# Kernel tuning notes

Hardware: AMD Instinct MI355X
Metric: run time of the kernel (lower is better)

Reference implementation:

```python
import jax, jax.numpy as jnp
import numpy as np

PADDING = 300
NMS_THRESH = 0.5


def bbox_transform_inv(boxes, deltas):
    # boxes: (N,4) x1,y1,x2,y2 ; deltas: (N,4*C) -> (N,4*C) decoded boxes
    w = boxes[:, 2] - boxes[:, 0] + 1.0
    h = boxes[:, 3] - boxes[:, 1] + 1.0
    cx = boxes[:, 0] + 0.5 * w
    cy = boxes[:, 1] + 0.5 * h
    dx, dy = deltas[:, 0::4], deltas[:, 1::4]
    dw, dh = deltas[:, 2::4], deltas[:, 3::4]
    pcx = dx * w[:, None] + cx[:, None]
    pcy = dy * h[:, None] + cy[:, None]
    pw = jnp.exp(dw) * w[:, None]
    ph = jnp.exp(dh) * h[:, None]
    out = jnp.stack([pcx - 0.5 * pw, pcy - 0.5 * ph,
                     pcx + 0.5 * pw, pcy + 0.5 * ph], axis=2)  # (N,C,4)
    return out.reshape(boxes.shape[0], -1)


def clip_boxes(boxes, hw):
    # hw = (H, W); boxes (N, 4*C)
    b = boxes.reshape(boxes.shape[0], -1, 4)
    x1 = jnp.clip(b[..., 0], 0.0, hw[1] - 1.0)
    y1 = jnp.clip(b[..., 1], 0.0, hw[0] - 1.0)
    x2 = jnp.clip(b[..., 2], 0.0, hw[1] - 1.0)
    y2 = jnp.clip(b[..., 3], 0.0, hw[0] - 1.0)
    return jnp.stack([x1, y1, x2, y2], axis=2).reshape(boxes.shape[0], -1)


def nms(boxes, scores, max_out, thresh):
    # Greedy NMS: sequential argmax + IoU suppression (fixed max_out iters).
    N = boxes.shape[0]
    x1, y1, x2, y2 = boxes[:, 0], boxes[:, 1], boxes[:, 2], boxes[:, 3]
    areas = (x2 - x1 + 1.0) * (y2 - y1 + 1.0)
    neg_inf = jnp.array(-jnp.inf, boxes.dtype)

    def step(s, _):
        i = jnp.argmax(s)
        valid = s[i] > neg_inf
        xx1 = jnp.maximum(x1[i], x1)
        yy1 = jnp.maximum(y1[i], y1)
        xx2 = jnp.minimum(x2[i], x2)
        yy2 = jnp.minimum(y2[i], y2)
        inter = jnp.maximum(xx2 - xx1 + 1.0, 0.0) * jnp.maximum(yy2 - yy1 + 1.0, 0.0)
        iou = inter / (areas[i] + areas - inter)
        suppress = (iou > thresh) | (jnp.arange(N) == i)
        s = jnp.where(suppress, neg_inf, s)
        return s, (i, valid)

    _, (idx, valid) = jax.lax.scan(step, scores, None, length=max_out)
    return idx, valid


def reference(metadata, deltas, proposals, scores, masks):
    N = proposals.shape[1]
    C = scores.shape[2]
    prop = proposals.reshape(-1, 4)
    boxes = prop / metadata[0, 2]                       # undo image scale
    d = deltas.reshape(N, -1)
    pred = bbox_transform_inv(boxes, d)                 # (N, 4C)
    pred = clip_boxes(pred, metadata[0, :2])
    sc = scores.reshape(N, C)
    top = jnp.argmax(sc, axis=1)                        # most probable class
    predc = pred.reshape(N, C, 4)
    pbox = jnp.take_along_axis(predc, top[:, None, None], axis=1)[:, 0, :]  # (N,4)
    max_scores = jnp.max(sc[:, 1:], axis=1)             # skip background col
    idx, valid = nms(jax.lax.stop_gradient(pbox),
                     jax.lax.stop_gradient(max_scores), PADDING, NMS_THRESH)
    vf = valid.astype(pbox.dtype)
    out_boxes = pbox[idx] * vf[:, None]                 # (300,4), zero padded
    out_scores = sc[idx] * vf[:, None]                  # (300,C)
    out_masks = masks[0][idx] * vf[:, None, None, None] # (300,mh,mw,mc)
    return out_boxes[None], out_scores[None], out_masks[None]


def setup_inputs() -> dict:
    key = jax.random.key(0)
    k1, k2, k3, k4, k5 = jax.random.split(key, 5)
    N, C, MH, MW, MC = 6000, 81, 14, 14, 81
    H, W, SCALE = 600.0, 800.0, 1.6
    metadata = jnp.array([[H, W, SCALE]], dtype=jnp.float32)
    # proposals: valid boxes inside the scaled image
    xy = jax.random.uniform(k1, (N, 2), jnp.float32) * jnp.array([W - 120.0, H - 120.0], jnp.float32)
    wh = jax.random.uniform(k2, (N, 2), jnp.float32) * 100.0 + 16.0
    proposals = jnp.concatenate([xy, xy + wh], axis=1)[None] * SCALE  # (1,N,4)
    deltas = jax.random.normal(k3, (1, N, 4 * C), jnp.float32) * 0.1
    scores = jax.random.uniform(k4, (1, N, C), jnp.float32)
    masks = jax.random.uniform(k5, (1, N, MH, MW, MC), jnp.float32)
    return {"metadata": metadata, "deltas": deltas, "proposals": proposals,
            "scores": scores, "masks": masks}
```

## Files before the change

### kernel.cpp

```cpp
#include <hip/hip_runtime.h>
#include <math.h>

#pragma STDC FP_CONTRACT OFF

#define N 6000
#define NPAD 6144
#define C 81
#define PADDING 300
#define NMS_THRESH 0.5f
#define MASK_ELEMS (14 * 14 * 81)
#define MASK_W 96
#define NCHUNK 8
#define CHUNK 750

typedef unsigned long long u64;

__global__ void decode_kernel(const float* __restrict__ meta,
                              const float* __restrict__ deltas,
                              const float* __restrict__ proposals,
                              const float* __restrict__ scores,
                              float* __restrict__ pbox,
                              float* __restrict__ area,
                              u64* __restrict__ skey) {
    int n = blockIdx.x * 4 + (threadIdx.x >> 6);
    int lane = threadIdx.x & 63;
    if (n >= N) return;

    const float* sr = scores + n * C;
    float s0 = sr[lane];
    float s1 = (lane < C - 64) ? sr[lane + 64] : -INFINITY;

    float av = s0;
    int ai = lane;
    if (s1 > av) { av = s1; ai = lane + 64; }
    float mv = (lane >= 1) ? s0 : -INFINITY;
    mv = fmaxf(mv, s1);

    for (int off = 32; off >= 1; off >>= 1) {
        float ov = __shfl_down(av, off);
        int oi = __shfl_down(ai, off);
        float om = __shfl_down(mv, off);
        if (ov > av || (ov == av && oi < ai)) { av = ov; ai = oi; }
        mv = fmaxf(mv, om);
    }

    if (lane == 0) {
        int top = ai;
        float ms = mv;

        float Hm = meta[0], Wm = meta[1], scale = meta[2];
        float b0 = proposals[n * 4 + 0] / scale;
        float b1 = proposals[n * 4 + 1] / scale;
        float b2 = proposals[n * 4 + 2] / scale;
        float b3 = proposals[n * 4 + 3] / scale;
        float w = b2 - b0 + 1.0f;
        float h = b3 - b1 + 1.0f;
        float cx = b0 + 0.5f * w;
        float cy = b1 + 0.5f * h;

        const float* dr = deltas + n * (4 * C) + 4 * top;
        float dx = dr[0], dy = dr[1], dw = dr[2], dh = dr[3];
        float pcx = dx * w + cx;
        float pcy = dy * h + cy;
        float pw = expf(dw) * w;
        float ph = expf(dh) * h;
        float x1 = pcx - 0.5f * pw;
        float y1 = pcy - 0.5f * ph;
        float x2 = pcx + 0.5f * pw;
        float y2 = pcy + 0.5f * ph;
        x1 = fminf(fmaxf(x1, 0.0f), Wm - 1.0f);
        y1 = fminf(fmaxf(y1, 0.0f), Hm - 1.0f);
        x2 = fminf(fmaxf(x2, 0.0f), Wm - 1.0f);
        y2 = fminf(fmaxf(y2, 0.0f), Hm - 1.0f);

        pbox[n * 4 + 0] = x1;
        pbox[n * 4 + 1] = y1;
        pbox[n * 4 + 2] = x2;
        pbox[n * 4 + 3] = y2;
        area[n] = (x2 - x1 + 1.0f) * (y2 - y1 + 1.0f);

        unsigned int b = __float_as_uint(ms);
        unsigned int u = b ^ ((b & 0x80000000u) ? 0xFFFFFFFFu : 0x80000000u);
        skey[n] = ((u64)u << 32) | (unsigned int)(~n);
    }
}

__global__ void rank_kernel(const u64* __restrict__ skey,
                            int* __restrict__ rank_part) {
    __shared__ u64 lk[CHUNK];
    int chunk = blockIdx.y;
    int t = threadIdx.x;
    int j0 = chunk * CHUNK;
    for (int j = t; j < CHUNK; j += 256) lk[j] = skey[j0 + j];
    __syncthreads();

    int i = blockIdx.x * 256 + t;
    if (i >= N) return;
    u64 mykey = skey[i];
    int cnt = 0;
    for (int j = 0; j < CHUNK; ++j) cnt += (lk[j] > mykey) ? 1 : 0;
    rank_part[chunk * NPAD + i] = cnt;
}

__global__ void scatter_kernel(const int* __restrict__ rank_part,
                               const float* __restrict__ pbox,
                               const float* __restrict__ area,
                               int* __restrict__ sidx,
                               float* __restrict__ sx1, float* __restrict__ sy1,
                               float* __restrict__ sx2, float* __restrict__ sy2,
                               float* __restrict__ sarea) {
    int i = blockIdx.x * blockDim.x + threadIdx.x;
    if (i >= N) return;
    int r = 0;
    for (int c = 0; c < NCHUNK; ++c) r += rank_part[c * NPAD + i];
    sidx[r] = i;
    sx1[r] = pbox[i * 4 + 0];
    sy1[r] = pbox[i * 4 + 1];
    sx2[r] = pbox[i * 4 + 2];
    sy2[r] = pbox[i * 4 + 3];
    sarea[r] = area[i];
}

__global__ void __launch_bounds__(256) iou_kernel(const float* __restrict__ sx1,
                                                  const float* __restrict__ sy1,
                                                  const float* __restrict__ sx2,
                                                  const float* __restrict__ sy2,
                                                  const float* __restrict__ sarea,
                                                  u64* __restrict__ mask) {
    int p = blockIdx.x * 4 + (threadIdx.x >> 6);
    int lane = threadIdx.x & 63;
    if (p >= N) return;

    float wx1 = sx1[p], wy1 = sy1[p], wx2 = sx2[p], wy2 = sy2[p];
    float war = sarea[p];
    u64* row = mask + (size_t)p * MASK_W;

    for (int w = (p >> 6); w < 94; ++w) {
        int q = w * 64 + lane;
        float xx1 = fmaxf(wx1, sx1[q]);
        float yy1 = fmaxf(wy1, sy1[q]);
        float xx2 = fminf(wx2, sx2[q]);
        float yy2 = fminf(wy2, sy2[q]);
        float inter = fmaxf(xx2 - xx1 + 1.0f, 0.0f) * fmaxf(yy2 - yy1 + 1.0f, 0.0f);
        float iou = inter / (war + sarea[q] - inter);
        u64 bal = __ballot(iou > NMS_THRESH);
        if (lane == 0) row[w] = bal;
    }
}

__device__ __forceinline__ void load_rows8(const u64* __restrict__ mask,
                                           int rowbase, int lane,
                                           u64* bx, u64* by) {
    if (lane < 48) {
#pragma unroll
        for (int k = 0; k < 8; ++k) {
            int r = rowbase + k;
            r = (r < N) ? r : (N - 1);
            const u64* q = mask + (size_t)r * MASK_W + 2 * lane;
            bx[k] = q[0];
            by[k] = q[1];
        }
    }
}

__global__ void scan_kernel(const u64* __restrict__ mask,
                            int* __restrict__ out_pos,
                            float* __restrict__ out_valid) {
    int lane = threadIdx.x;
    int w0 = 2 * lane, w1 = 2 * lane + 1;

    u64 m_lo = (w0 < 93) ? 0ULL : (w0 == 93 ? 0xFFFF000000000000ULL : ~0ULL);
    u64 m_hi = (w1 < 93) ? 0ULL : (w1 == 93 ? 0xFFFF000000000000ULL : ~0ULL);

    u64 ax[8], ay[8], bx[8], by[8];
#pragma unroll
    for (int k = 0; k < 8; ++k) { ax[k] = 0; ay[k] = 0; bx[k] = 0; by[k] = 0; }

    int base = 0;
    load_rows8(mask, 0, lane, ax, ay);
    load_rows8(mask, 8, lane, bx, by);

    int r = 0;
    while (r < PADDING) {
        u64 z0 = ~m_lo, z1 = ~m_hi;
        u64 bal = __ballot((z0 | z1) != 0ULL);
        if (bal == 0ULL) break;
        int lsrc = (int)__ffsll(bal) - 1;
        int local = (z0 != 0ULL) ? ((int)__ffsll(z0) - 1) : (64 + (int)__ffsll(z1) - 1);
        int p = __builtin_amdgcn_readlane(lane * 128 + local, lsrc);

        if (p >= base + 16) {
            base = p;
            load_rows8(mask, base, lane, ax, ay);
            load_rows8(mask, base + 8, lane, bx, by);
        } else if (p >= base + 8) {
            base += 8;
#pragma unroll
            for (int k = 0; k < 8; ++k) { ax[k] = bx[k]; ay[k] = by[k]; }
            load_rows8(mask, base + 8, lane, bx, by);
        }
        int s = p - base;
        u64 vx = ax[0], vy = ay[0];
#pragma unroll
        for (int k = 1; k < 8; ++k) {
            if (s == k) { vx = ax[k]; vy = ay[k]; }
        }
        if (lane < 48) { m_lo |= vx; m_hi |= vy; }
        if (lane == 0) { out_pos[r] = p; out_valid[r] = 1.0f; }
        ++r;
    }
    for (; r < PADDING; ++r) {
        if (lane == 0) { out_pos[r] = 0; out_valid[r] = 0.0f; }
    }
}

__global__ void gather_kernel(const float* __restrict__ pbox,
                              const float* __restrict__ scores,
                              const float* __restrict__ masks,
                              const int* __restrict__ sidx,
                              const int* __restrict__ out_pos,
                              const float* __restrict__ valid,
                              float* __restrict__ out) {
    int b = blockIdx.x;
    int tid = threadIdx.x;
    int i = sidx[out_pos[b]];
    float vf = valid[b];

    if (tid < 4) out[b * 4 + tid] = pbox[i * 4 + tid] * vf;
    if (tid < C) out[PADDING * 4 + b * C + tid] = scores[i * C + tid] * vf;

    const float4* src = (const float4*)(masks + (size_t)i * MASK_ELEMS);
    float4* dst = (float4*)(out + PADDING * 4 + PADDING * C + (size_t)b * MASK_ELEMS);
    for (int m = tid; m < MASK_ELEMS / 4; m += 256) {
        float4 v = src[m];
        dst[m] = make_float4(v.x * vf, v.y * vf, v.z * vf, v.w * vf);
    }
}

extern "C" void kernel_launch(void* const* d_in, const int* in_sizes, int n_in,
                              void* d_out, int out_size, void* d_ws, size_t ws_size,
                              hipStream_t stream) {
    const float* meta      = (const float*)d_in[0];
    const float* deltas    = (const float*)d_in[1];
    const float* proposals = (const float*)d_in[2];
    const float* scores    = (const float*)d_in[3];
    const float* masks     = (const float*)d_in[4];
    float* out = (float*)d_out;

    char* ws = (char*)d_ws;
    u64*   mask      = (u64*)(ws);
    u64*   skey      = (u64*)(ws + 4608000);
    float* pbox      = (float*)(ws + 4657152);
    float* area      = (float*)(ws + 4753152);
    int*   rank_part = (int*)(ws + 4777152);
    int*   sidx      = (int*)(ws + 4973760);
    float* sx1       = (float*)(ws + 4998336);
    float* sy1       = (float*)(ws + 5022912);
    float* sx2       = (float*)(ws + 5047488);
    float* sy2       = (float*)(ws + 5072064);
    float* sarea     = (float*)(ws + 5096640);
    int*   out_pos   = (int*)(ws + 5121216);
    float* out_valid = (float*)(ws + 5122416);

    decode_kernel<<<1500, 256, 0, stream>>>(meta, deltas, proposals, scores, pbox, area, skey);
    rank_kernel<<<dim3(24, NCHUNK), 256, 0, stream>>>(skey, rank_part);
    scatter_kernel<<<24, 256, 0, stream>>>(rank_part, pbox, area, sidx, sx1, sy1, sx2, sy2, sarea);
    iou_kernel<<<1500, 256, 0, stream>>>(sx1, sy1, sx2, sy2, sarea, mask);
    scan_kernel<<<1, 64, 0, stream>>>(mask, out_pos, out_valid);
    gather_kernel<<<PADDING, 256, 0, stream>>>(pbox, scores, masks, sidx, out_pos, out_valid, out);
}
```

Measured before the change: 602.5 us.

## Prefetch suppression-mask rows for next eight candidates in NMS scan

Replaces the block-of-16 row buffering in the serial NMS scan with a rotating queue of eight prefetched mask rows, one per upcoming unsuppressed candidate, found via a first-zero-after search. Each pop checks whether the queued candidate was killed by later merges and, if not, ORs its row into the mask. A new row load is issued eight steps ahead, hiding global-load latency on the sequential critical path. Queued candidates that are suppressed in the meantime cost a wasted load and an extra iteration.

```diff
diff --git a/kernel.cpp b/kernel.cpp
--- a/kernel.cpp
+++ b/kernel.cpp
@@ -12,6 +12,7 @@
 #define MASK_W 96
 #define NCHUNK 8
 #define CHUNK 750
+#define ZSENT 0x40000000
 
 typedef unsigned long long u64;
 
@@ -148,19 +149,20 @@
     }
 }
 
-__device__ __forceinline__ void load_rows8(const u64* __restrict__ mask,
-                                           int rowbase, int lane,
-                                           u64* bx, u64* by) {
-    if (lane < 48) {
-#pragma unroll
-        for (int k = 0; k < 8; ++k) {
-            int r = rowbase + k;
-            r = (r < N) ? r : (N - 1);
-            const u64* q = mask + (size_t)r * MASK_W + 2 * lane;
-            bx[k] = q[0];
-            by[k] = q[1];
-        }
-    }
+__device__ __forceinline__ int first_zero_ge(u64 m_lo, u64 m_hi, int lane, int start) {
+    u64 z0 = ~m_lo, z1 = ~m_hi;
+    int b0 = (2 * lane) << 6;
+    int s0 = start - b0;
+    if (s0 > 0) z0 = (s0 >= 64) ? 0ULL : (z0 & (~0ULL << s0));
+    int s1 = s0 - 64;
+    if (s1 > 0) z1 = (s1 >= 64) ? 0ULL : (z1 & (~0ULL << s1));
+    int local = -1;
+    if (z0) local = (int)__ffsll(z0) - 1;
+    else if (z1) local = 64 + (int)__ffsll(z1) - 1;
+    u64 bal = __ballot(local >= 0);
+    if (bal == 0ULL) return ZSENT;
+    int lsrc = (int)__ffsll(bal) - 1;
+    return __builtin_amdgcn_readlane(lane * 128 + local, lsrc);
 }
 
 __global__ void scan_kernel(const u64* __restrict__ mask,
@@ -172,43 +174,64 @@
     u64 m_lo = (w0 < 93) ? 0ULL : (w0 == 93 ? 0xFFFF000000000000ULL : ~0ULL);
     u64 m_hi = (w1 < 93) ? 0ULL : (w1 == 93 ? 0xFFFF000000000000ULL : ~0ULL);
 
-    u64 ax[8], ay[8], bx[8], by[8];
-#pragma unroll
-    for (int k = 0; k < 8; ++k) { ax[k] = 0; ay[k] = 0; bx[k] = 0; by[k] = 0; }
-
-    int base = 0;
-    load_rows8(mask, 0, lane, ax, ay);
-    load_rows8(mask, 8, lane, bx, by);
+    int zq0 = 0, zq1 = 1, zq2 = 2, zq3 = 3, zq4 = 4, zq5 = 5, zq6 = 6, zq7 = 7;
+    ulonglong2 rq0, rq1, rq2, rq3, rq4, rq5, rq6, rq7;
+    rq0.x = rq0.y = rq1.x = rq1.y = rq2.x = rq2.y = rq3.x = rq3.y = 0ULL;
+    rq4.x = rq4.y = rq5.x = rq5.y = rq6.x = rq6.y = rq7.x = rq7.y = 0ULL;
+    if (lane < 48) {
+        const u64* mb = mask + 2 * lane;
+        rq0 = *(const ulonglong2*)(mb + (size_t)0 * MASK_W);
+        rq1 = *(const ulonglong2*)(mb + (size_t)1 * MASK_W);
+        rq2 = *(const ulonglong2*)(mb + (size_t)2 * MASK_W);
+        rq3 = *(const ulonglong2*)(mb + (size_t)3 * MASK_W);
+        rq4 = *(const ulonglong2*)(mb + (size_t)4 * MASK_W);
+        rq5 = *(const ulonglong2*)(mb + (size_t)5 * MASK_W);
+        rq6 = *(const ulonglong2*)(mb + (size_t)6 * MASK_W);
+        rq7 = *(const ulonglong2*)(mb + (size_t)7 * MASK_W);
+    }
 
     int r = 0;
-    while (r < PADDING) {
-        u64 z0 = ~m_lo, z1 = ~m_hi;
-        u64 bal = __ballot((z0 | z1) != 0ULL);
-        if (bal == 0ULL) break;
-        int lsrc = (int)__ffsll(bal) - 1;
-        int local = (z0 != 0ULL) ? ((int)__ffsll(z0) - 1) : (64 + (int)__ffsll(z1) - 1);
-        int p = __builtin_amdgcn_readlane(lane * 128 + local, lsrc);
-
-        if (p >= base + 16) {
-            base = p;
-            load_rows8(mask, base, lane, ax, ay);
-            load_rows8(mask, base + 8, lane, bx, by);
-        } else if (p >= base + 8) {
-            base += 8;
-#pragma unroll
-            for (int k = 0; k < 8; ++k) { ax[k] = bx[k]; ay[k] = by[k]; }
-            load_rows8(mask, base + 8, lane, bx, by);
-        }
-        int s = p - base;
-        u64 vx = ax[0], vy = ay[0];
-#pragma unroll
-        for (int k = 1; k < 8; ++k) {
-            if (s == k) { vx = ax[k]; vy = ay[k]; }
-        }
-        if (lane < 48) { m_lo |= vx; m_hi |= vy; }
-        if (lane == 0) { out_pos[r] = p; out_valid[r] = 1.0f; }
-        ++r;
-    }
+    bool done = false;
+
+#define POP(RQ)                                                               \
+    {                                                                         \
+        int z0h = zq0;                                                        \
+        if (z0h >= N || r >= PADDING) {                                       \
+            done = true;                                                      \
+        } else {                                                              \
+            int wdi = z0h >> 6;                                  \
+            u64 wsel = (wdi & 1) ? m_hi : m_lo;                               \
+            unsigned bit = (unsigned)((wsel >> (z0h & 63)) & 1ULL);           \
+            unsigned killed =                                                 \
+                (unsigned)__builtin_amdgcn_readlane((int)bit, wdi >> 1);      \
+            if (!killed) {                                                    \
+                if (lane < 48) { m_lo |= RQ.x; m_hi |= RQ.y; }                \
+                if (lane == 0) { out_pos[r] = z0h; out_valid[r] = 1.0f; }     \
+                ++r;                                                          \
+            }                                                                 \
+            int nstart = zq7 + 1;                                             \
+            zq0 = zq1; zq1 = zq2; zq2 = zq3; zq3 = zq4;                       \
+            zq4 = zq5; zq5 = zq6; zq6 = zq7;                                  \
+            int nz = first_zero_ge(m_lo, m_hi, lane, nstart);                 \
+            zq7 = nz;                                                         \
+            int lr = (nz < N) ? nz : 0;                                       \
+            if (lane < 48)                                                    \
+                RQ = *(const ulonglong2*)(mask + (size_t)lr * MASK_W + 2 * lane); \
+        }                                                                     \
+    }
+
+    while (!done) {
+        POP(rq0); if (done) break;
+        POP(rq1); if (done) break;
+        POP(rq2); if (done) break;
+        POP(rq3); if (done) break;
+        POP(rq4); if (done) break;
+        POP(rq5); if (done) break;
+        POP(rq6); if (done) break;
+        POP(rq7);
+    }
+#undef POP
+
     for (; r < PADDING; ++r) {
         if (lane == 0) { out_pos[r] = 0; out_valid[r] = 0.0f; }
     }
```

Result: no change. 609.2 us (+1.1%).
